# Optimization experiments

Hardware: AMD Instinct MI355X
Metric: run time of the kernel (lower is better)

Reference implementation:

```python
import jax, jax.numpy as jnp
import numpy as np


def setup_inputs() -> dict:
    key = jax.random.key(0)
    k1, k2 = jax.random.split(key)
    K, D = 8192, 256
    z_e_x = jax.random.normal(k1, (4, D, 32, 64), dtype=jnp.float32)
    # matches uniform(-1/K, 1/K) init scale-wise, but any values work for correctness
    codebook = jax.random.uniform(k2, (K, D), dtype=jnp.float32, minval=-1.0 / K, maxval=1.0 / K)
    return {"z_e_x": z_e_x, "codebook": codebook}


def reference(z_e_x, codebook):
    b, D, h, t = z_e_x.shape
    K = codebook.shape[0]
    # permute to channels-last and flatten: [b*h*t, D]
    x = jnp.transpose(z_e_x, (0, 2, 3, 1)).reshape(-1, D)
    x_sqr = jnp.sum(x * x, axis=1, keepdims=True)          # [N, 1]
    c_sqr = jnp.sum(codebook * codebook, axis=1)           # [K]
    distances = x_sqr + c_sqr - 2.0 * jnp.einsum('nd,kd->nk', x, codebook)
    indices = jnp.argmin(distances, axis=1)                # [N] int
    # gather quantized codes and restore [b, D, h, t] layout
    z_q_x_bar = jnp.transpose(codebook[indices].reshape(b, h, t, D), (0, 3, 1, 2))
    # commitment loss: 0.25 * mse(z_e_x, stop_grad(z_q_x_bar))
    commitment_loss = 0.25 * jnp.mean((z_e_x - jax.lax.stop_gradient(z_q_x_bar)) ** 2)
    return indices.reshape(b, h, t), z_q_x_bar, commitment_loss
```

## Files before the change

kernel.cpp:

```cpp
#include <hip/hip_runtime.h>
#include <hip/hip_bf16.h>
#include <cstdint>
#include <cstddef>


#define NPTS 8192
#define KCB  8192

typedef __attribute__((ext_vector_type(4))) float f32x4;

#define X_OFF    0u
#define XB8_OFF  8388608u
#define CB8_OFF  10485760u
#define CSQ_OFF  12582912u
#define XSQP_OFF 12615680u
#define CNT_OFF  12877824u
#define CAND_OFF 12910592u
#define PART_OFF 15007744u

__device__ __forceinline__ void gld_lds16(const void* g, void* l) {
  __builtin_amdgcn_global_load_lds(
      (const __attribute__((address_space(1))) void*)g,
      (__attribute__((address_space(3))) void*)l, 16, 0, 0);
}

__global__ __launch_bounds__(256) void prep_k(
    const float* __restrict__ z, const float* __restrict__ cb,
    float* __restrict__ x, unsigned char* __restrict__ xb8,
    unsigned char* __restrict__ cb8, float* __restrict__ csq,
    float* __restrict__ xsqp, unsigned int* __restrict__ cnt) {
  int blk = blockIdx.x;
  int tid = threadIdx.x;
  if (blk < 2048) {
    __shared__ float tile[32][33];
    int mb = blk & 63, db = (blk >> 6) & 7, b = blk >> 9;
    int m0 = mb * 32, d0 = db * 32;
    int tx = tid & 31, ty = tid >> 5;
    const float* inb = z + (size_t)b * 524288;
    #pragma unroll
    for (int j = 0; j < 4; ++j)
      tile[ty + j*8][tx] = inb[(size_t)(d0 + ty + j*8) * 2048 + m0 + tx];
    __syncthreads();
    int mm = tid >> 3, dg = tid & 7;
    float v0 = tile[dg*4+0][mm], v1 = tile[dg*4+1][mm];
    float v2 = tile[dg*4+2][mm], v3 = tile[dg*4+3][mm];
    int n = b * 2048 + m0 + mm;
    float4 f4 = {v0, v1, v2, v3};
    *(float4*)&x[(size_t)n * 256 + d0 + dg * 4] = f4;
    unsigned int pk = __builtin_amdgcn_cvt_pk_fp8_f32(v0, v1, 0, 0);
    pk = __builtin_amdgcn_cvt_pk_fp8_f32(v2, v3, pk, 1);
    *(unsigned int*)&xb8[(size_t)n * 256 + d0 + dg * 4] = pk;
    float s = v0*v0 + v1*v1 + v2*v2 + v3*v3;
    s += __shfl_xor(s, 1); s += __shfl_xor(s, 2); s += __shfl_xor(s, 4);
    if (dg == 0) xsqp[db * 8192 + n] = s;
  } else {
    int blk2 = blk - 2048;
    int wave = tid >> 6, lane = tid & 63;
    int row = blk2 * 4 + wave;
    float4 v = *(const float4*)&cb[(size_t)row * 256 + lane * 4];
    unsigned int pk = __builtin_amdgcn_cvt_pk_fp8_f32(v.x * 8192.f, v.y * 8192.f, 0, 0);
    pk = __builtin_amdgcn_cvt_pk_fp8_f32(v.z * 8192.f, v.w * 8192.f, pk, 1);
    *(unsigned int*)&cb8[(size_t)row * 256 + lane * 4] = pk;
    float s = v.x*v.x + v.y*v.y + v.z*v.z + v.w*v.w;
    #pragma unroll
    for (int off = 32; off > 0; off >>= 1) s += __shfl_xor(s, off);
    if (lane == 0) csq[row] = s;
    if (tid < 4) cnt[blk2 * 4 + tid] = 0u;
  }
}

__global__ __launch_bounds__(256, 4) void gemm_filter_k(
    const unsigned char* __restrict__ xb8, const unsigned char* __restrict__ cb8,
    const float* __restrict__ xsqp, unsigned int* __restrict__ cnt,
    int* __restrict__ cand) {
  __shared__ unsigned char smemB[4][2][4096];
  __shared__ int cand_s[64][20];
  __shared__ int ccnt_s[64];
  __shared__ float thr_s[64];
  const int tid = threadIdx.x;
  const int lane = tid & 63, w = tid >> 6;
  const int wn = w >> 1, wk = w & 1;
  const int half = lane >> 4;
  const int qr   = lane & 15;
  const int n0 = blockIdx.x * 64;
  const int kbase = blockIdx.y * 1024 + wk * 512;

  if (tid < 64) {
    float xs = 0.f;
    #pragma unroll
    for (int db = 0; db < 8; ++db) xs += xsqp[db * 8192 + n0 + tid];
    thr_s[tid] = 1.6455f * sqrtf(xs);
    ccnt_s[tid] = 0;
  }
  __syncthreads();

  long long a[2][8];
  #pragma unroll
  for (int i = 0; i < 2; ++i) {
    int arow = n0 + wn * 32 + i * 16 + qr;
    #pragma unroll
    for (int ds = 0; ds < 8; ++ds)
      a[i][ds] = *(const long long*)&xb8[(size_t)arow * 256 + ds * 32 + half * 8];
  }
  float thv[2][4], thmin[2];
  #pragma unroll
  for (int i = 0; i < 2; ++i) {
    #pragma unroll
    for (int r = 0; r < 4; ++r)
      thv[i][r] = thr_s[wn * 32 + i * 16 + half * 4 + r];
    thmin[i] = fminf(fminf(thv[i][0], thv[i][1]), fminf(thv[i][2], thv[i][3]));
  }
  asm volatile("s_waitcnt vmcnt(0)" ::: "memory");

#define STAGE_B(p_, cc_) do {                                                  \
    _Pragma("unroll")                                                          \
    for (int q = 0; q < 4; ++q) {                                              \
      int cw_ = q * 4 + (lane >> 4);                  \
      int src_ = ((2 * (lane & 15)) ^ (cw_ << 1)) * 8;                         \
      gld_lds16(&cb8[(size_t)(kbase + (cc_) * 16 + cw_) * 256 + src_],         \
                &smemB[w][p_][q * 1024]);                                      \
    }                                                                          \
  } while (0)

#define FOLD(av_, i_, kv_) do {                                                \
    float mx_ = fmaxf(fmaxf(av_[0], av_[1]), fmaxf(av_[2], av_[3]));           \
    if (mx_ > thmin[i_]) {                                                     \
      _Pragma("unroll")                                                        \
      for (int r = 0; r < 4; ++r) {                                            \
        if (av_[r] > thv[i_][r]) {                                             \
          int rloc_ = wn * 32 + (i_) * 16 + half * 4 + r;                      \
          int pos_ = atomicAdd(&ccnt_s[rloc_], 1);                             \
          if (pos_ < 20) cand_s[rloc_][pos_] = (kv_);                          \
        }                                                                      \
      }                                                                        \
    }                                                                          \
  } while (0)

#define ITER(cc_, p_, vm_) do {                                                \
    asm volatile("s_waitcnt vmcnt(" #vm_ ")" ::: "memory");                    \
    __builtin_amdgcn_sched_barrier(0);                                         \
    __builtin_amdgcn_s_setprio(1);                                             \
    f32x4 acc0 = zz, acc1 = zz;                                                \
    _Pragma("unroll")                                                          \
    for (int ds = 0; ds < 8; ++ds) {                                           \
      long long b = *(const long long*)                                        \
          &smemB[w][p_][qr * 256 + (((ds * 4 + half) ^ (qr << 1))) * 8];       \
      acc0 = __builtin_amdgcn_mfma_f32_16x16x32_fp8_fp8(a[0][ds], b, acc0, 0, 0, 0); \
      acc1 = __builtin_amdgcn_mfma_f32_16x16x32_fp8_fp8(a[1][ds], b, acc1, 0, 0, 0); \
    }                                                                          \
    __builtin_amdgcn_s_setprio(0);                                             \
    asm volatile("s_waitcnt lgkmcnt(0)" ::: "memory");     \
    if ((cc_) + 2 < 32) STAGE_B(p_, (cc_) + 2);                                \
    int kv = kbase + (cc_) * 16 + qr;                                          \
    FOLD(acc0, 0, kv); FOLD(acc1, 1, kv);                                      \
  } while (0)

  const f32x4 zz = {0.f, 0.f, 0.f, 0.f};
  STAGE_B(0, 0);
  STAGE_B(1, 1);
  #pragma unroll 1
  for (int c = 0; c < 30; c += 2) {
    ITER(c, 0, 4);
    ITER(c + 1, 1, 4);
  }
  ITER(30, 0, 4);
  ITER(31, 1, 0);
#undef STAGE_B
#undef ITER
#undef FOLD

  __syncthreads();
  if (tid < 64) {
    int local = ccnt_s[tid];
    int stored = local < 20 ? local : 20;
    unsigned int add = (unsigned int)stored + (local > 20 ? 0x100000u : 0u);
    unsigned int base = atomicAdd(&cnt[n0 + tid], add);
    for (int i2 = 0; i2 < stored; ++i2) {
      unsigned int p = base + (unsigned int)i2;
      if (p < 64u) cand[(size_t)(n0 + tid) * 64 + p] = cand_s[tid][i2];
    }
  }
}

__global__ __launch_bounds__(256) void rescore_k(
    const float* __restrict__ x, const float* __restrict__ cb,
    const float* __restrict__ csq, const float* __restrict__ xsqp,
    const unsigned int* __restrict__ cnt, const int* __restrict__ cand,
    float* __restrict__ outIdx) {
  __shared__ float xrow[256];
  __shared__ float sv[16];
  __shared__ int sk[16];
  __shared__ float xsp_s[8];
  __shared__ float xs_sh;
  int n = blockIdx.x, tid = threadIdx.x;
  int g = tid >> 4, l = tid & 15;
  if (tid < 8) xsp_s[tid] = xsqp[tid * 8192 + n];
  xrow[tid] = x[(size_t)n * 256 + tid];
  __syncthreads();
  if (tid == 0) {
    float s = 0.f;
    #pragma unroll
    for (int db = 0; db < 8; ++db) s += xsp_s[db];
    xs_sh = s;
  }
  __syncthreads();
  unsigned int raw = cnt[n];
  bool fb = (raw == 0u) || (raw > 64u);
  int M = fb ? KCB : (int)raw;
  float xs = xs_sh;
  float bs = 3.4e38f; int bk = 0x7fffffff;
  for (int c = g; c < M; c += 16) {
    int k = fb ? c : cand[n * 64 + c];
    const float* cr = cb + (size_t)k * 256;
    float dot = 0.f;
    #pragma unroll
    for (int j = 0; j < 16; ++j) dot = fmaf(xrow[j * 16 + l], cr[j * 16 + l], dot);
    #pragma unroll
    for (int off = 1; off < 16; off <<= 1) dot += __shfl_xor(dot, off);
    float s = (xs + csq[k]) - 2.0f * dot;
    if (s < bs || (s == bs && k < bk)) { bs = s; bk = k; }
  }
  if (l == 0) { sv[g] = bs; sk[g] = bk; }
  __syncthreads();
  if (tid == 0) {
    #pragma unroll
    for (int u = 1; u < 16; ++u)
      if (sv[u] < bs || (sv[u] == bs && sk[u] < bk)) { bs = sv[u]; bk = sk[u]; }
    outIdx[n] = (float)bk;
  }
}

__global__ void gather_k(const float* __restrict__ zin, const float* __restrict__ cb,
                         const float* __restrict__ outIdx, float* __restrict__ zq,
                         float* __restrict__ part) {
  __shared__ float red[256];
  int tid = threadIdx.x;
  int g = (blockIdx.x * 256 + tid) * 4;
  int b = g >> 19;
  int rem = g & 524287;
  int d = rem >> 11;
  int m = rem & 2047;
  int nb = b * 2048 + m;
  float4 z4 = *(const float4*)&zin[g];
  float4 i4 = *(const float4*)&outIdx[nb];
  float za[4] = {z4.x, z4.y, z4.z, z4.w};
  float ia[4] = {i4.x, i4.y, i4.z, i4.w};
  float4 c4;
  float* ca = (float*)&c4;
  float s = 0.f;
  #pragma unroll
  for (int u = 0; u < 4; ++u) {
    int idx = (int)ia[u];
    float c = cb[(size_t)idx * 256 + d];
    ca[u] = c;
    float diff = za[u] - c;
    s += diff * diff;
  }
  *(float4*)&zq[g] = c4;
  red[tid] = s;
  __syncthreads();
  for (int s2 = 128; s2 > 0; s2 >>= 1) {
    if (tid < s2) red[tid] += red[tid + s2];
    __syncthreads();
  }
  if (tid == 0) part[blockIdx.x] = red[0];
}

__global__ void loss_k(const float* __restrict__ part, float* __restrict__ outLoss) {
  __shared__ float red[256];
  int tid = threadIdx.x;
  float s = 0.f;
  for (int r = 0; r < 8; ++r) s += part[tid + r * 256];
  red[tid] = s;
  __syncthreads();
  for (int s2 = 128; s2 > 0; s2 >>= 1) {
    if (tid < s2) red[tid] += red[tid + s2];
    __syncthreads();
  }
  if (tid == 0) outLoss[0] = 0.25f * red[0] / 2097152.0f;
}

extern "C" void kernel_launch(void* const* d_in, const int* in_sizes, int n_in,
                              void* d_out, int out_size, void* d_ws, size_t ws_size,
                              hipStream_t stream) {
  const float* z  = (const float*)d_in[0];
  const float* cb = (const float*)d_in[1];
  float* out = (float*)d_out;
  char* ws = (char*)d_ws;
  float* x            = (float*)(ws + X_OFF);
  unsigned char* xb8  = (unsigned char*)(ws + XB8_OFF);
  unsigned char* cb8  = (unsigned char*)(ws + CB8_OFF);
  float* csq          = (float*)(ws + CSQ_OFF);
  float* xsqp         = (float*)(ws + XSQP_OFF);
  unsigned int* cnt   = (unsigned int*)(ws + CNT_OFF);
  int* cand           = (int*)(ws + CAND_OFF);
  float* part         = (float*)(ws + PART_OFF);

  prep_k<<<4096, 256, 0, stream>>>(z, cb, x, xb8, cb8, csq, xsqp, cnt);
  gemm_filter_k<<<dim3(128, 8), 256, 0, stream>>>(xb8, cb8, xsqp, cnt, cand);
  rescore_k<<<NPTS, 256, 0, stream>>>(x, cb, csq, xsqp, cnt, cand, out);
  gather_k<<<2048, 256, 0, stream>>>(z, cb, out, out + 8192, part);
  loss_k<<<1, 256, 0, stream>>>(part, out + 8192 + 2097152);
}
```

Measured before the change: 82.45 us.

## Move threshold compute to separate kernel and write candidates directly to global

Per-point thresholds are now computed in a small separate kernel. The GEMM filter no longer computes them and drops its shared-memory candidate buffers and the end-of-block flush, appending candidates with global atomics instead. With less LDS per block the launch bound is raised to 5 blocks per CU to gain occupancy. The cost is an extra launch and contended global atomics, and the overflow marker plus per-block cap of 20 candidates are gone. prep_k also writes thr from cb blocks that may read xsqp before it is ready, but thr_k overwrites it.

```diff
diff --git a/kernel.cpp b/kernel.cpp
--- a/kernel.cpp
+++ b/kernel.cpp
@@ -17,6 +17,7 @@
 #define CNT_OFF  12877824u
 #define CAND_OFF 12910592u
 #define PART_OFF 15007744u
+#define THR_OFF  15015936u
 
 __device__ __forceinline__ void gld_lds16(const void* g, void* l) {
   __builtin_amdgcn_global_load_lds(
@@ -28,11 +29,13 @@
     const float* __restrict__ z, const float* __restrict__ cb,
     float* __restrict__ x, unsigned char* __restrict__ xb8,
     unsigned char* __restrict__ cb8, float* __restrict__ csq,
-    float* __restrict__ xsqp, unsigned int* __restrict__ cnt) {
+    float* __restrict__ xsqp, unsigned int* __restrict__ cnt,
+    float* __restrict__ thr) {
   int blk = blockIdx.x;
   int tid = threadIdx.x;
   if (blk < 2048) {
     __shared__ float tile[32][33];
+    __shared__ float xsq_t[32];
     int mb = blk & 63, db = (blk >> 6) & 7, b = blk >> 9;
     int m0 = mb * 32, d0 = db * 32;
     int tx = tid & 31, ty = tid >> 5;
@@ -66,17 +69,30 @@
     for (int off = 32; off > 0; off >>= 1) s += __shfl_xor(s, off);
     if (lane == 0) csq[row] = s;
     if (tid < 4) cnt[blk2 * 4 + tid] = 0u;
-  }
-}
-
-__global__ __launch_bounds__(256, 4) void gemm_filter_k(
+    if (tid < 4) {
+      int n = blk2 * 4 + tid;
+      float xs = 0.f;
+      #pragma unroll
+      for (int db = 0; db < 8; ++db) xs += xsqp[db * 8192 + n];
+      thr[n] = 1.6455f * sqrtf(xs);
+    }
+  }
+}
+
+__global__ __launch_bounds__(256) void thr_k(const float* __restrict__ xsqp,
+                                             float* __restrict__ thr) {
+  int n = blockIdx.x * 256 + threadIdx.x;
+  float xs = 0.f;
+  #pragma unroll
+  for (int db = 0; db < 8; ++db) xs += xsqp[db * 8192 + n];
+  thr[n] = 1.6455f * sqrtf(xs);
+}
+
+__global__ __launch_bounds__(256, 5) void gemm_filter_k(
     const unsigned char* __restrict__ xb8, const unsigned char* __restrict__ cb8,
-    const float* __restrict__ xsqp, unsigned int* __restrict__ cnt,
+    const float* __restrict__ thr, unsigned int* __restrict__ cnt,
     int* __restrict__ cand) {
   __shared__ unsigned char smemB[4][2][4096];
-  __shared__ int cand_s[64][20];
-  __shared__ int ccnt_s[64];
-  __shared__ float thr_s[64];
   const int tid = threadIdx.x;
   const int lane = tid & 63, w = tid >> 6;
   const int wn = w >> 1, wk = w & 1;
@@ -85,15 +101,6 @@
   const int n0 = blockIdx.x * 64;
   const int kbase = blockIdx.y * 1024 + wk * 512;
 
-  if (tid < 64) {
-    float xs = 0.f;
-    #pragma unroll
-    for (int db = 0; db < 8; ++db) xs += xsqp[db * 8192 + n0 + tid];
-    thr_s[tid] = 1.6455f * sqrtf(xs);
-    ccnt_s[tid] = 0;
-  }
-  __syncthreads();
-
   long long a[2][8];
   #pragma unroll
   for (int i = 0; i < 2; ++i) {
@@ -107,7 +114,7 @@
   for (int i = 0; i < 2; ++i) {
     #pragma unroll
     for (int r = 0; r < 4; ++r)
-      thv[i][r] = thr_s[wn * 32 + i * 16 + half * 4 + r];
+      thv[i][r] = thr[n0 + wn * 32 + i * 16 + half * 4 + r];
     thmin[i] = fminf(fminf(thv[i][0], thv[i][1]), fminf(thv[i][2], thv[i][3]));
   }
   asm volatile("s_waitcnt vmcnt(0)" ::: "memory");
@@ -128,9 +135,9 @@
       _Pragma("unroll")                                                        \
       for (int r = 0; r < 4; ++r) {                                            \
         if (av_[r] > thv[i_][r]) {                                             \
-          int rloc_ = wn * 32 + (i_) * 16 + half * 4 + r;                      \
-          int pos_ = atomicAdd(&ccnt_s[rloc_], 1);                             \
-          if (pos_ < 20) cand_s[rloc_][pos_] = (kv_);                          \
+          int n_ = n0 + wn * 32 + (i_) * 16 + half * 4 + r;                    \
+          unsigned int pos_ = atomicAdd(&cnt[n_], 1u);                         \
+          if (pos_ < 64u) cand[(size_t)n_ * 64 + pos_] = (kv_);                \
         }                                                                      \
       }                                                                        \
     }                                                                          \
@@ -168,18 +175,6 @@
 #undef STAGE_B
 #undef ITER
 #undef FOLD
-
-  __syncthreads();
-  if (tid < 64) {
-    int local = ccnt_s[tid];
-    int stored = local < 20 ? local : 20;
-    unsigned int add = (unsigned int)stored + (local > 20 ? 0x100000u : 0u);
-    unsigned int base = atomicAdd(&cnt[n0 + tid], add);
-    for (int i2 = 0; i2 < stored; ++i2) {
-      unsigned int p = base + (unsigned int)i2;
-      if (p < 64u) cand[(size_t)(n0 + tid) * 64 + p] = cand_s[tid][i2];
-    }
-  }
 }
 
 __global__ __launch_bounds__(256) void rescore_k(
@@ -295,9 +290,11 @@
   unsigned int* cnt   = (unsigned int*)(ws + CNT_OFF);
   int* cand           = (int*)(ws + CAND_OFF);
   float* part         = (float*)(ws + PART_OFF);
-
-  prep_k<<<4096, 256, 0, stream>>>(z, cb, x, xb8, cb8, csq, xsqp, cnt);
-  gemm_filter_k<<<dim3(128, 8), 256, 0, stream>>>(xb8, cb8, xsqp, cnt, cand);
+  float* thr          = (float*)(ws + THR_OFF);
+
+  prep_k<<<4096, 256, 0, stream>>>(z, cb, x, xb8, cb8, csq, xsqp, cnt, thr);
+  thr_k<<<32, 256, 0, stream>>>(xsqp, thr);
+  gemm_filter_k<<<dim3(128, 8), 256, 0, stream>>>(xb8, cb8, thr, cnt, cand);
   rescore_k<<<NPTS, 256, 0, stream>>>(x, cb, csq, xsqp, cnt, cand, out);
   gather_k<<<2048, 256, 0, stream>>>(z, cb, out, out + 8192, part);
   loss_k<<<1, 256, 0, stream>>>(part, out + 8192 + 2097152);
```

After: 106.9 us. 29.6% more time.
